# Kernel optimization log

Measured on AMD Instinct MI355X. Metric: run time of the kernel, lower is better.

## Reference

```python
import jax, jax.numpy as jnp
import numpy as np

F, V, E = 26, 100000, 16          # fields, vocab per field, embedding dim
CONT, H1, H2 = 13, 400, 400
B = 16384


def setup_inputs() -> dict:
    key = jax.random.key(0)
    ks = jax.random.split(key, 12)
    dnn_in_dim = CONT + F * E  # 429
    return {
        "continuous": jax.random.normal(ks[0], (B, CONT), jnp.float32),
        "categorical": jax.random.randint(ks[1], (B, F), 0, V, jnp.int32),
        "w_cont": jax.random.normal(ks[2], (CONT, 1), jnp.float32) * 0.05,
        "b_cont": jnp.zeros((1,), jnp.float32),
        "tables_first": jax.random.normal(ks[3], (F, V, 1), jnp.float32) * 0.05,
        "tables_emb": jax.random.normal(ks[4], (F, V, E), jnp.float32) * 0.05,
        "W1": jax.random.normal(ks[5], (dnn_in_dim, H1), jnp.float32) * 0.05,
        "b1": jnp.zeros((H1,), jnp.float32),
        "W2": jax.random.normal(ks[6], (H1, H2), jnp.float32) * 0.05,
        "b2": jnp.zeros((H2,), jnp.float32),
        "W_out": jax.random.normal(ks[7], (H2 + 1, 1), jnp.float32) * 0.05,
        "b_out": jnp.zeros((1,), jnp.float32),
    }


def reference(continuous, categorical, w_cont, b_cont, tables_first, tables_emb,
              W1, b1, W2, b2, W_out, b_out):
    # per-field gather: tables [F,V,D], categorical [B,F] -> [B,F,D]
    gather = jax.vmap(lambda tab, idx: tab[idx], in_axes=(0, 1), out_axes=1)
    # ---- FM first order ----
    first = gather(tables_first, categorical)            # [B, F, 1]
    fm1 = continuous @ w_cont + b_cont + jnp.sum(first, axis=1)  # [B, 1]
    # ---- FM second order (sum-square trick) ----
    emb = gather(tables_emb, categorical)                # [B, F, E]
    sum_emb = jnp.sum(emb, axis=1)                       # [B, E]
    sum_square = jnp.sum(jnp.square(emb), axis=1)        # [B, E]
    fm2 = 0.5 * jnp.sum(jnp.square(sum_emb) - sum_square, axis=1, keepdims=True)
    fm_out = fm1 + fm2                                   # [B, 1]
    # ---- DNN (dropout is identity at inference) ----
    dnn_in = jnp.concatenate([continuous, emb.reshape(emb.shape[0], -1)], axis=1)
    h = jax.nn.relu(dnn_in @ W1 + b1)
    h = jax.nn.relu(h @ W2 + b2)
    fusion = jnp.concatenate([fm_out, h], axis=1)        # [B, 1+H2]
    return fusion @ W_out + b_out                        # [B, 1]
```

## Files before the change

kernel.cpp:

```cpp
#include <hip/hip_runtime.h>

typedef unsigned short ushort_t;
typedef unsigned int uint_t;

__device__ __forceinline__ float bf2f(ushort_t u) {
    union { float f; uint_t i; } c; c.i = ((uint_t)u) << 16; return c.f;
}
__device__ __forceinline__ ushort_t f2bf(float f) {
    union { float f; uint_t i; } c; c.f = f;
    uint_t i = c.i;
    return (ushort_t)((i + 0x7fffu + ((i >> 16) & 1u)) >> 16);
}

typedef __attribute__((ext_vector_type(8))) short short8;
typedef __attribute__((ext_vector_type(4))) float float4v;

#define BATCH 16384
#define NV    100000
#define NPAD  448
#define K1    480
#define K2    416
#define ROWS  32
#define SA    488
#define SH    456

#define OFF_W1T 0u
#define OFF_W2T 430080u

__global__ void prep_weights(const float* __restrict__ W1, const float* __restrict__ W2,
                             ushort_t* __restrict__ W1t, ushort_t* __restrict__ W2t) {
    int i = blockIdx.x * 256 + threadIdx.x;
    if (i < NPAD * K1) {
        int n = i / K1, k = i % K1;
        ushort_t o = 0;
        if (n < 400) {
            if (k < 416) {
                o = f2bf(W1[(size_t)(13 + k) * 400 + n]);
            } else if (k < 448) {
                int j = k - (k < 432 ? 416 : 432);
                if (j < 13) o = f2bf(W1[(size_t)j * 400 + n]);
            } else if (k < 464) {
                int j = k - 448;
                if (j < 13) {
                    float wv = W1[(size_t)j * 400 + n];
                    ushort_t wh = f2bf(wv);
                    o = f2bf(wv - bf2f(wh));
                }
            }
        }
        W1t[i] = o;
    } else {
        int j = i - NPAD * K1;
        if (j < NPAD * K2) {
            int n = j / K2, k = j % K2;
            W2t[j] = (n < 400 && k < 400) ? f2bf(W2[(size_t)k * 400 + n]) : (ushort_t)0;
        }
    }
}

__global__ __launch_bounds__(256, 2) void fused_deepfm(
    const float* __restrict__ cont, const int* __restrict__ cat,
    const float* __restrict__ w_cont, const float* __restrict__ b_cont,
    const float* __restrict__ t_first, const float* __restrict__ t_emb,
    const ushort_t* __restrict__ W1t, const float* __restrict__ b1,
    const ushort_t* __restrict__ W2t, const float* __restrict__ b2,
    const float* __restrict__ Wout, const float* __restrict__ bout,
    float* __restrict__ out)
{
    __shared__ __align__(16) ushort_t smA[ROWS * SA];
    __shared__ float smFM[ROWS];
    __shared__ float smP[4 * ROWS];

    int tid  = threadIdx.x;
    int wv   = tid >> 6, lane = tid & 63;
    int quad = lane >> 4, mrow = lane & 15;
    int b0   = blockIdx.x * ROWS;
    ushort_t* smH = smA;

    {
        int r4 = lane >> 4, fs = (lane >> 2) & 3, sub = lane & 3, l16 = lane & 15;
        int idxv[2][7];
        #pragma unroll
        for (int g = 0; g < 2; ++g) {
            int gR = b0 + wv * 8 + g * 4 + r4;
            #pragma unroll
            for (int it = 0; it < 7; ++it) {
                int f = it * 4 + fs;
                idxv[g][it] = (f < 26) ? cat[gR * 26 + f] : 0;
            }
        }
        #pragma unroll
        for (int g = 0; g < 2; ++g) {
            int R  = wv * 8 + g * 4 + r4;
            int gR = b0 + R;
            float sj0 = 0, sj1 = 0, sj2 = 0, sj3 = 0, ssq = 0, pacc = 0;
            #pragma unroll
            for (int it = 0; it < 7; ++it) {
                int f = it * 4 + fs;
                if (f < 26) {
                    int idx = idxv[g][it];
                    const float* ep = t_emb + (((size_t)f * NV + idx) << 4) + sub * 4;
                    float4 v = *(const float4*)ep;
                    sj0 += v.x; sj1 += v.y; sj2 += v.z; sj3 += v.w;
                    ssq += v.x * v.x + v.y * v.y + v.z * v.z + v.w * v.w;
                    uint_t lo = (uint_t)f2bf(v.x) | ((uint_t)f2bf(v.y) << 16);
                    uint_t hi = (uint_t)f2bf(v.z) | ((uint_t)f2bf(v.w) << 16);
                    uint2 pk = make_uint2(lo, hi);
                    *(uint2*)&smA[R * SA + f * 16 + sub * 4] = pk;
                    if (sub == 0) pacc += t_first[(size_t)f * NV + idx];
                }
            }
            float c = (l16 < 13) ? cont[gR * 13 + l16] : 0.f;
            if (l16 < 13) pacc += c * w_cont[l16];
            ushort_t ch = f2bf(c);
            float cl = c - bf2f(ch);
            smA[R * SA + 416 + l16] = ch;
            smA[R * SA + 432 + l16] = f2bf(cl);
            smA[R * SA + 448 + l16] = ch;
            smA[R * SA + 464 + l16] = 0;
            sj0 += __shfl_xor(sj0, 4); sj0 += __shfl_xor(sj0, 8);
            sj1 += __shfl_xor(sj1, 4); sj1 += __shfl_xor(sj1, 8);
            sj2 += __shfl_xor(sj2, 4); sj2 += __shfl_xor(sj2, 8);
            sj3 += __shfl_xor(sj3, 4); sj3 += __shfl_xor(sj3, 8);
            float q = pacc - 0.5f * ssq;
            if (fs == 0) q += 0.5f * (sj0 * sj0 + sj1 * sj1 + sj2 * sj2 + sj3 * sj3);
            q += __shfl_xor(q, 1); q += __shfl_xor(q, 2);
            q += __shfl_xor(q, 4); q += __shfl_xor(q, 8);
            if (l16 == 0) smFM[R] = q + b_cont[0];
        }
    }
    __syncthreads();

    int n0 = wv * 7;

    {
        const ushort_t* Bb = W1t + (size_t)mrow * K1 + quad * 8;
        short8 bcur[7], bnxt[7];
        #pragma unroll
        for (int ni = 0; ni < 7; ++ni)
            bcur[ni] = *(const short8*)(Bb + (size_t)(n0 + ni) * 16 * K1);
        float4v acc[2][7] = {};
        #pragma unroll 1
        for (int s = 0; s < 15; ++s) {
            if (s < 14) {
                #pragma unroll
                for (int ni = 0; ni < 7; ++ni)
                    bnxt[ni] = *(const short8*)(Bb + (size_t)(n0 + ni) * 16 * K1 + (s + 1) * 32);
            }
            short8 af[2];
            #pragma unroll
            for (int mt = 0; mt < 2; ++mt)
                af[mt] = *(const short8*)&smA[(mt * 16 + mrow) * SA + s * 32 + quad * 8];
            #pragma unroll
            for (int ni = 0; ni < 7; ++ni)
                #pragma unroll
                for (int mt = 0; mt < 2; ++mt)
                    acc[mt][ni] = __builtin_amdgcn_mfma_f32_16x16x32_bf16(af[mt], bcur[ni], acc[mt][ni], 0, 0, 0);
            #pragma unroll
            for (int ni = 0; ni < 7; ++ni) bcur[ni] = bnxt[ni];
        }
        __syncthreads();
        #pragma unroll
        for (int ni = 0; ni < 7; ++ni) {
            int col = n0 * 16 + ni * 16 + mrow;
            float bv = (col < 400) ? b1[col] : 0.f;
            #pragma unroll
            for (int mt = 0; mt < 2; ++mt)
                #pragma unroll
                for (int r = 0; r < 4; ++r) {
                    int row = mt * 16 + quad * 4 + r;
                    smH[row * SH + col] = f2bf(fmaxf(acc[mt][ni][r] + bv, 0.f));
                }
        }
    }
    __syncthreads();

    {
        const ushort_t* Bb = W2t + (size_t)mrow * K2 + quad * 8;
        short8 bcur[7], bnxt[7];
        #pragma unroll
        for (int ni = 0; ni < 7; ++ni)
            bcur[ni] = *(const short8*)(Bb + (size_t)(n0 + ni) * 16 * K2);
        float4v acc[2][7] = {};
        #pragma unroll 1
        for (int s = 0; s < 13; ++s) {
            if (s < 12) {
                #pragma unroll
                for (int ni = 0; ni < 7; ++ni)
                    bnxt[ni] = *(const short8*)(Bb + (size_t)(n0 + ni) * 16 * K2 + (s + 1) * 32);
            }
            short8 af[2];
            #pragma unroll
            for (int mt = 0; mt < 2; ++mt)
                af[mt] = *(const short8*)&smH[(mt * 16 + mrow) * SH + s * 32 + quad * 8];
            #pragma unroll
            for (int ni = 0; ni < 7; ++ni)
                #pragma unroll
                for (int mt = 0; mt < 2; ++mt)
                    acc[mt][ni] = __builtin_amdgcn_mfma_f32_16x16x32_bf16(af[mt], bcur[ni], acc[mt][ni], 0, 0, 0);
            #pragma unroll
            for (int ni = 0; ni < 7; ++ni) bcur[ni] = bnxt[ni];
        }
        float p[2][4] = {};
        #pragma unroll
        for (int ni = 0; ni < 7; ++ni) {
            int col = n0 * 16 + ni * 16 + mrow;
            if (col < 400) {
                float bv = b2[col], wvv = Wout[1 + col];
                #pragma unroll
                for (int mt = 0; mt < 2; ++mt)
                    #pragma unroll
                    for (int r = 0; r < 4; ++r)
                        p[mt][r] += fmaxf(acc[mt][ni][r] + bv, 0.f) * wvv;
            }
        }
        #pragma unroll
        for (int mt = 0; mt < 2; ++mt)
            #pragma unroll
            for (int r = 0; r < 4; ++r) {
                float v = p[mt][r];
                v += __shfl_xor(v, 1); v += __shfl_xor(v, 2);
                v += __shfl_xor(v, 4); v += __shfl_xor(v, 8);
                p[mt][r] = v;
            }
        if (mrow == 0) {
            #pragma unroll
            for (int mt = 0; mt < 2; ++mt)
                #pragma unroll
                for (int r = 0; r < 4; ++r)
                    smP[wv * ROWS + mt * 16 + quad * 4 + r] = p[mt][r];
        }
    }
    __syncthreads();

    if (tid < ROWS) {
        float o = smP[tid] + smP[ROWS + tid] + smP[2 * ROWS + tid] + smP[3 * ROWS + tid];
        out[b0 + tid] = o + smFM[tid] * Wout[0] + bout[0];
    }
}

extern "C" void kernel_launch(void* const* d_in, const int* in_sizes, int n_in,
                              void* d_out, int out_size, void* d_ws, size_t ws_size,
                              hipStream_t stream) {
    const float* cont    = (const float*)d_in[0];
    const int*   cat     = (const int*)d_in[1];
    const float* w_cont  = (const float*)d_in[2];
    const float* b_cont  = (const float*)d_in[3];
    const float* t_first = (const float*)d_in[4];
    const float* t_emb   = (const float*)d_in[5];
    const float* W1      = (const float*)d_in[6];
    const float* b1      = (const float*)d_in[7];
    const float* W2      = (const float*)d_in[8];
    const float* b2      = (const float*)d_in[9];
    const float* Wout    = (const float*)d_in[10];
    const float* bout    = (const float*)d_in[11];
    float* out = (float*)d_out;

    char* w = (char*)d_ws;
    ushort_t* W1t = (ushort_t*)(w + OFF_W1T);
    ushort_t* W2t = (ushort_t*)(w + OFF_W2T);

    prep_weights<<<1568, 256, 0, stream>>>(W1, W2, W1t, W2t);
    fused_deepfm<<<BATCH / ROWS, 256, 0, stream>>>(cont, cat, w_cont, b_cont,
                                                   t_first, t_emb, W1t, b1, W2t, b2,
                                                   Wout, bout, out);
}
```

Before: 275.7 us.

## Pre-swizzle weights into MFMA fragment order and skip padded column tiles

```diff
diff --git a/kernel.cpp b/kernel.cpp
--- a/kernel.cpp
+++ b/kernel.cpp
@@ -17,43 +17,45 @@
 
 #define BATCH 16384
 #define NV    100000
-#define NPAD  448
 #define K1    480
 #define K2    416
+#define NT    25
+#define S1    15
+#define S2    13
 #define ROWS  32
 #define SA    488
 #define SH    456
 
-#define OFF_W1T 0u
-#define OFF_W2T 430080u
+#define OFF_W1F 0u
+#define OFF_W2F 384000u
 
 __global__ void prep_weights(const float* __restrict__ W1, const float* __restrict__ W2,
-                             ushort_t* __restrict__ W1t, ushort_t* __restrict__ W2t) {
+                             ushort_t* __restrict__ W1f, ushort_t* __restrict__ W2f) {
     int i = blockIdx.x * 256 + threadIdx.x;
-    if (i < NPAD * K1) {
+    if (i < 400 * K1) {
         int n = i / K1, k = i % K1;
         ushort_t o = 0;
-        if (n < 400) {
-            if (k < 416) {
-                o = f2bf(W1[(size_t)(13 + k) * 400 + n]);
-            } else if (k < 448) {
-                int j = k - (k < 432 ? 416 : 432);
-                if (j < 13) o = f2bf(W1[(size_t)j * 400 + n]);
-            } else if (k < 464) {
-                int j = k - 448;
-                if (j < 13) {
-                    float wv = W1[(size_t)j * 400 + n];
-                    ushort_t wh = f2bf(wv);
-                    o = f2bf(wv - bf2f(wh));
-                }
-            }
-        }
-        W1t[i] = o;
+        if (k < 416) {
+            o = f2bf(W1[(size_t)(13 + k) * 400 + n]);
+        } else if (k < 448) {
+            int j = k - (k < 432 ? 416 : 432);
+            if (j < 13) o = f2bf(W1[(size_t)j * 400 + n]);
+        } else if (k < 464) {
+            int j = k - 448;
+            if (j < 13) {
+                float wv = W1[(size_t)j * 400 + n];
+                o = f2bf(wv - bf2f(f2bf(wv)));
+            }
+        }
+        int t = n >> 4, mr = n & 15, s = k >> 5, q = (k >> 3) & 3, j = k & 7;
+        W1f[(size_t)((t * S1 + s) * 64 + q * 16 + mr) * 8 + j] = o;
     } else {
-        int j = i - NPAD * K1;
-        if (j < NPAD * K2) {
-            int n = j / K2, k = j % K2;
-            W2t[j] = (n < 400 && k < 400) ? f2bf(W2[(size_t)k * 400 + n]) : (ushort_t)0;
+        int i2 = i - 400 * K1;
+        if (i2 < 400 * K2) {
+            int n = i2 / K2, k = i2 % K2;
+            ushort_t o = (k < 400) ? f2bf(W2[(size_t)k * 400 + n]) : (ushort_t)0;
+            int t = n >> 4, mr = n & 15, s = k >> 5, q = (k >> 3) & 3, j = k & 7;
+            W2f[(size_t)((t * S2 + s) * 64 + q * 16 + mr) * 8 + j] = o;
         }
     }
 }
@@ -62,8 +64,8 @@
     const float* __restrict__ cont, const int* __restrict__ cat,
     const float* __restrict__ w_cont, const float* __restrict__ b_cont,
     const float* __restrict__ t_first, const float* __restrict__ t_emb,
-    const ushort_t* __restrict__ W1t, const float* __restrict__ b1,
-    const ushort_t* __restrict__ W2t, const float* __restrict__ b2,
+    const ushort_t* __restrict__ W1f, const float* __restrict__ b1,
+    const ushort_t* __restrict__ W2f, const float* __restrict__ b2,
     const float* __restrict__ Wout, const float* __restrict__ bout,
     float* __restrict__ out)
 {
@@ -76,6 +78,7 @@
     int quad = lane >> 4, mrow = lane & 15;
     int b0   = blockIdx.x * ROWS;
     ushort_t* smH = smA;
+    const int ntiles = (wv < 3) ? 7 : 4;
 
     {
         int r4 = lane >> 4, fs = (lane >> 2) & 3, sub = lane & 3, l16 = lane & 15;
@@ -131,21 +134,19 @@
     }
     __syncthreads();
 
-    int n0 = wv * 7;
-
     {
-        const ushort_t* Bb = W1t + (size_t)mrow * K1 + quad * 8;
+        const ushort_t* Bb = W1f + (size_t)(wv * 7 * S1) * 512 + lane * 8;
         short8 bcur[7], bnxt[7];
         #pragma unroll
         for (int ni = 0; ni < 7; ++ni)
-            bcur[ni] = *(const short8*)(Bb + (size_t)(n0 + ni) * 16 * K1);
+            if (ni < ntiles) bcur[ni] = *(const short8*)(Bb + (size_t)(ni * S1) * 512);
         float4v acc[2][7] = {};
         #pragma unroll 1
-        for (int s = 0; s < 15; ++s) {
-            if (s < 14) {
+        for (int s = 0; s < S1; ++s) {
+            if (s < S1 - 1) {
                 #pragma unroll
                 for (int ni = 0; ni < 7; ++ni)
-                    bnxt[ni] = *(const short8*)(Bb + (size_t)(n0 + ni) * 16 * K1 + (s + 1) * 32);
+                    if (ni < ntiles) bnxt[ni] = *(const short8*)(Bb + (size_t)(ni * S1 + s + 1) * 512);
             }
             short8 af[2];
             #pragma unroll
@@ -153,41 +154,50 @@
                 af[mt] = *(const short8*)&smA[(mt * 16 + mrow) * SA + s * 32 + quad * 8];
             #pragma unroll
             for (int ni = 0; ni < 7; ++ni)
+                if (ni < ntiles)
+                    #pragma unroll
+                    for (int mt = 0; mt < 2; ++mt)
+                        acc[mt][ni] = __builtin_amdgcn_mfma_f32_16x16x32_bf16(af[mt], bcur[ni], acc[mt][ni], 0, 0, 0);
+            #pragma unroll
+            for (int ni = 0; ni < 7; ++ni) bcur[ni] = bnxt[ni];
+        }
+        __syncthreads();
+        #pragma unroll
+        for (int ni = 0; ni < 7; ++ni)
+            if (ni < ntiles) {
+                int col = (wv * 7 + ni) * 16 + mrow;
+                float bv = b1[col];
                 #pragma unroll
                 for (int mt = 0; mt < 2; ++mt)
-                    acc[mt][ni] = __builtin_amdgcn_mfma_f32_16x16x32_bf16(af[mt], bcur[ni], acc[mt][ni], 0, 0, 0);
-            #pragma unroll
-            for (int ni = 0; ni < 7; ++ni) bcur[ni] = bnxt[ni];
-        }
-        __syncthreads();
-        #pragma unroll
-        for (int ni = 0; ni < 7; ++ni) {
-            int col = n0 * 16 + ni * 16 + mrow;
-            float bv = (col < 400) ? b1[col] : 0.f;
-            #pragma unroll
-            for (int mt = 0; mt < 2; ++mt)
-                #pragma unroll
-                for (int r = 0; r < 4; ++r) {
-                    int row = mt * 16 + quad * 4 + r;
-                    smH[row * SH + col] = f2bf(fmaxf(acc[mt][ni][r] + bv, 0.f));
-                }
+                    #pragma unroll
+                    for (int r = 0; r < 4; ++r) {
+                        int row = mt * 16 + quad * 4 + r;
+                        smH[row * SH + col] = f2bf(fmaxf(acc[mt][ni][r] + bv, 0.f));
+                    }
+            }
+        if (wv == 3) {
+            #pragma unroll
+            for (int mt = 0; mt < 2; ++mt)
+                #pragma unroll
+                for (int r = 0; r < 4; ++r)
+                    smH[(mt * 16 + quad * 4 + r) * SH + 400 + mrow] = 0;
         }
     }
     __syncthreads();
 
     {
-        const ushort_t* Bb = W2t + (size_t)mrow * K2 + quad * 8;
+        const ushort_t* Bb = W2f + (size_t)(wv * 7 * S2) * 512 + lane * 8;
         short8 bcur[7], bnxt[7];
         #pragma unroll
         for (int ni = 0; ni < 7; ++ni)
-            bcur[ni] = *(const short8*)(Bb + (size_t)(n0 + ni) * 16 * K2);
+            if (ni < ntiles) bcur[ni] = *(const short8*)(Bb + (size_t)(ni * S2) * 512);
         float4v acc[2][7] = {};
         #pragma unroll 1
-        for (int s = 0; s < 13; ++s) {
-            if (s < 12) {
+        for (int s = 0; s < S2; ++s) {
+            if (s < S2 - 1) {
                 #pragma unroll
                 for (int ni = 0; ni < 7; ++ni)
-                    bnxt[ni] = *(const short8*)(Bb + (size_t)(n0 + ni) * 16 * K2 + (s + 1) * 32);
+                    if (ni < ntiles) bnxt[ni] = *(const short8*)(Bb + (size_t)(ni * S2 + s + 1) * 512);
             }
             short8 af[2];
             #pragma unroll
@@ -195,17 +205,18 @@
                 af[mt] = *(const short8*)&smH[(mt * 16 + mrow) * SH + s * 32 + quad * 8];
             #pragma unroll
             for (int ni = 0; ni < 7; ++ni)
-                #pragma unroll
-                for (int mt = 0; mt < 2; ++mt)
-                    acc[mt][ni] = __builtin_amdgcn_mfma_f32_16x16x32_bf16(af[mt], bcur[ni], acc[mt][ni], 0, 0, 0);
+                if (ni < ntiles)
+                    #pragma unroll
+                    for (int mt = 0; mt < 2; ++mt)
+                        acc[mt][ni] = __builtin_amdgcn_mfma_f32_16x16x32_bf16(af[mt], bcur[ni], acc[mt][ni], 0, 0, 0);
             #pragma unroll
             for (int ni = 0; ni < 7; ++ni) bcur[ni] = bnxt[ni];
         }
         float p[2][4] = {};
         #pragma unroll
-        for (int ni = 0; ni < 7; ++ni) {
-            int col = n0 * 16 + ni * 16 + mrow;
-            if (col < 400) {
+        for (int ni = 0; ni < 7; ++ni)
+            if (ni < ntiles) {
+                int col = (wv * 7 + ni) * 16 + mrow;
                 float bv = b2[col], wvv = Wout[1 + col];
                 #pragma unroll
                 for (int mt = 0; mt < 2; ++mt)
@@ -213,7 +224,6 @@
                     for (int r = 0; r < 4; ++r)
                         p[mt][r] += fmaxf(acc[mt][ni][r] + bv, 0.f) * wvv;
             }
-        }
         #pragma unroll
         for (int mt = 0; mt < 2; ++mt)
             #pragma unroll
@@ -257,11 +267,11 @@
     float* out = (float*)d_out;
 
     char* w = (char*)d_ws;
-    ushort_t* W1t = (ushort_t*)(w + OFF_W1T);
-    ushort_t* W2t = (ushort_t*)(w + OFF_W2T);
-
-    prep_weights<<<1568, 256, 0, stream>>>(W1, W2, W1t, W2t);
+    ushort_t* W1f = (ushort_t*)(w + OFF_W1F);
+    ushort_t* W2f = (ushort_t*)(w + OFF_W2F);
+
+    prep_weights<<<1400, 256, 0, stream>>>(W1, W2, W1f, W2f);
     fused_deepfm<<<BATCH / ROWS, 256, 0, stream>>>(cont, cat, w_cont, b_cont,
-                                                   t_first, t_emb, W1t, b1, W2t, b2,
+                                                   t_first, t_emb, W1f, b1, W2f, b2,
                                                    Wout, bout, out);
 }
```

New measurement: 265.9 us. 1.04x faster.
